# Optimization experiments

Measured on AMD Instinct MI355X. Metric: run time of the kernel, lower is better.

## Reference

```python
import jax, jax.numpy as jnp
import numpy as np

N_VAR, N_CONS = 100_000, 50_000
N_FEAS = N_VAR + N_CONS
E_OBJ, E_FEAS = 1_600_000, 2_400_000
H_OBJ = H_CONS = 64
C = H_OBJ + H_CONS  # concat_dim = 128
D = 256             # decoder_hidden_channels
NUM_GRAPHS = 64


def _gcn(x, src, dst, ew, W, b):
    # PyG GCNConv with edge weights: add self-loops (weight 1), sym-normalize, aggregate at dst.
    n = x.shape[0]
    loop = jnp.arange(n)
    src_f = jnp.concatenate([src, loop])
    dst_f = jnp.concatenate([dst, loop])
    ew_f = jnp.concatenate([ew, jnp.ones((n,), ew.dtype)])
    deg = jax.ops.segment_sum(ew_f, dst_f, num_segments=n)
    dinv = jnp.where(deg > 0, jax.lax.rsqrt(deg), 0.0)
    coef = dinv[src_f] * ew_f * dinv[dst_f]            # [E+n]
    h = x @ W                                          # [n, H]
    out = jax.ops.segment_sum(coef[:, None] * h[src_f], dst_f, num_segments=n)
    return out + b


def _mlp(z, W1, b1, W2, b2):
    return jnp.maximum(z @ W1 + b1, 0.0) @ W2 + b2


def setup_inputs() -> dict:
    key = jax.random.key(0)
    ks = iter(jax.random.split(key, 64))

    def nrm(shape, scale=1.0):
        return jax.random.normal(next(ks), shape, jnp.float32) * scale

    def lin(i, o):
        return nrm((i, o), 1.0 / np.sqrt(i)), jnp.zeros((o,), jnp.float32)

    inp = {}
    inp['x_obj'] = nrm((N_VAR, 4))
    inp['ei_obj'] = jax.random.randint(next(ks), (2, E_OBJ), 0, N_VAR)
    inp['ew_obj'] = jax.random.uniform(next(ks), (E_OBJ,), jnp.float32)
    inp['x_feas'] = nrm((N_FEAS, 4))
    inp['ei_feas'] = jax.random.randint(next(ks), (2, E_FEAS), 0, N_FEAS)
    inp['ew_feas'] = jax.random.uniform(next(ks), (E_FEAS,), jnp.float32)
    inp['batch_var'] = jnp.sort(jax.random.randint(next(ks), (N_VAR,), 0, NUM_GRAPHS))
    inp['n_var'] = N_VAR
    inp['n_bin'] = 50_000
    inp['c1o_W'], inp['c1o_b'] = lin(4, H_OBJ)
    inp['c2o_W'], inp['c2o_b'] = lin(H_OBJ, H_OBJ)
    inp['c1c_W'], inp['c1c_b'] = lin(4, H_CONS)
    inp['c2c_W'], inp['c2c_b'] = lin(H_CONS, H_CONS)
    inp['mu_W'], inp['mu_b'] = lin(C, C)
    inp['lv_W'], inp['lv_b'] = lin(C, C)
    inp['dx_W1'], inp['dx_b1'] = lin(C, D)
    inp['dx_W2'], inp['dx_b2'] = lin(D, 1)
    inp['dc_W1'], inp['dc_b1'] = lin(C, D)
    inp['dc_W2'], inp['dc_b2'] = lin(D, 1)
    inp['dk_W1'], inp['dk_b1'] = lin(C, D)
    inp['dk_W2'], inp['dk_b2'] = lin(D, 1)
    inp['di_W1'], inp['di_b1'] = lin(C, D)
    inp['di_W2'], inp['di_b2'] = lin(D, 1)
    return inp


def reference(x_obj, ei_obj, ew_obj, x_feas, ei_feas, ew_feas, batch_var, n_var, n_bin,
              c1o_W, c1o_b, c2o_W, c2o_b, c1c_W, c1c_b, c2c_W, c2c_b,
              mu_W, mu_b, lv_W, lv_b,
              dx_W1, dx_b1, dx_W2, dx_b2, dc_W1, dc_b1, dc_W2, dc_b2,
              dk_W1, dk_b1, dk_W2, dk_b2, di_W1, di_b1, di_W2, di_b2):
    so, do = ei_obj[0], ei_obj[1]
    sf, df = ei_feas[0], ei_feas[1]
    # objective encoder (all nodes are variables)
    h = jax.nn.relu(_gcn(x_obj, so, do, ew_obj, c1o_W, c1o_b))
    z_obj_var = jax.nn.relu(_gcn(h, so, do, ew_obj, c2o_W, c2o_b))
    # constraints encoder
    h = jax.nn.relu(_gcn(x_feas, sf, df, ew_feas, c1c_W, c1c_b))
    h = jax.nn.relu(_gcn(h, sf, df, ew_feas, c2c_W, c2c_b))
    z_cons_var = h[:n_var]          # variable_mask == first n_var nodes
    z_cons_constraints = h[n_var:]
    z_var = jnp.concatenate([z_obj_var, z_cons_var], axis=1)        # [N_var, C]
    z_cons_pad = jnp.pad(z_cons_constraints, ((0, 0), (0, C - z_cons_constraints.shape[1])))
    z_shared = jnp.concatenate([z_var, z_cons_pad], axis=0)         # [N_feas, C]
    z_mu = z_shared @ mu_W + mu_b
    z_logvar = z_shared @ lv_W + lv_b
    eps = jax.random.normal(jax.random.key(1), z_mu.shape, z_mu.dtype)
    z = z_mu + jnp.exp(0.5 * z_logvar) * eps
    z_var_s = z[:n_var]
    z_con_s = z[n_var:]
    x_hat = _mlp(z_var_s, dx_W1, dx_b1, dx_W2, dx_b2)[:, 0]
    # global_mean_pool over variable nodes
    sums = jax.ops.segment_sum(z_var_s, batch_var, num_segments=NUM_GRAPHS)
    cnts = jax.ops.segment_sum(jnp.ones((z_var_s.shape[0],), z.dtype), batch_var, num_segments=NUM_GRAPHS)
    pooled = sums / jnp.maximum(cnts, 1.0)[:, None]
    predicted_cost = _mlp(pooled, dc_W1, dc_b1, dc_W2, dc_b2)[:, 0]
    predicted_constraints = _mlp(z_con_s, dk_W1, dk_b1, dk_W2, dk_b2)[:, 0]
    integrality = jax.nn.sigmoid(_mlp(z_var_s, di_W1, di_b1, di_W2, di_b2))[:, 0]
    predicted_integrality = integrality[:n_bin]  # binary_mask == first n_bin variables
    return (x_hat, predicted_cost, predicted_constraints, predicted_integrality, z_mu, z_logvar)
```

## Files before the change

### kernel.cpp

```cpp
#include <hip/hip_runtime.h>
#include <math.h>

#define N_VAR_C  100000
#define N_CONS_C 50000
#define N_FEAS_C 150000
#define E_OBJ_C  1600000
#define E_FEAS_C 2400000
#define NG 64
#define N_BIN_C 50000
#define CAP 48

#define X_HAT_OFF 0
#define COST_OFF  100000
#define CONS_OFF  100064
#define INTG_OFF  150064
#define ZMU_OFF   200064
#define ZEL_TOTAL (N_FEAS_C * 128)
#define ZLV_OFF   (ZMU_OFF + ZEL_TOTAL)

typedef unsigned short u16;

static __device__ __forceinline__ float bf2f(u16 u) {
  return __uint_as_float(((unsigned)u) << 16);
}
static __device__ __forceinline__ u16 f2bf(float f) {
  unsigned x = __float_as_uint(f);
  unsigned r = x + 0x7FFFu + ((x >> 16) & 1u);
  return (u16)(r >> 16);
}

static __device__ __forceinline__ unsigned rotl32(unsigned x, unsigned r) {
  return (x << r) | (x >> (32u - r));
}

static __device__ __forceinline__ void threefry01(unsigned x0, unsigned x1,
                                                  unsigned& o0, unsigned& o1) {
  const unsigned ks0 = 0u, ks1 = 1u, ks2 = 0x1BD11BDAu ^ 0u ^ 1u;
  x0 += ks0; x1 += ks1;
  x0 += x1; x1 = rotl32(x1, 13); x1 ^= x0;
  x0 += x1; x1 = rotl32(x1, 15); x1 ^= x0;
  x0 += x1; x1 = rotl32(x1, 26); x1 ^= x0;
  x0 += x1; x1 = rotl32(x1, 6);  x1 ^= x0;
  x0 += ks1; x1 += ks2 + 1u;
  x0 += x1; x1 = rotl32(x1, 17); x1 ^= x0;
  x0 += x1; x1 = rotl32(x1, 29); x1 ^= x0;
  x0 += x1; x1 = rotl32(x1, 16); x1 ^= x0;
  x0 += x1; x1 = rotl32(x1, 24); x1 ^= x0;
  x0 += ks2; x1 += ks0 + 2u;
  x0 += x1; x1 = rotl32(x1, 13); x1 ^= x0;
  x0 += x1; x1 = rotl32(x1, 15); x1 ^= x0;
  x0 += x1; x1 = rotl32(x1, 26); x1 ^= x0;
  x0 += x1; x1 = rotl32(x1, 6);  x1 ^= x0;
  x0 += ks0; x1 += ks1 + 3u;
  x0 += x1; x1 = rotl32(x1, 17); x1 ^= x0;
  x0 += x1; x1 = rotl32(x1, 29); x1 ^= x0;
  x0 += x1; x1 = rotl32(x1, 16); x1 ^= x0;
  x0 += x1; x1 = rotl32(x1, 24); x1 ^= x0;
  x0 += ks1; x1 += ks2 + 4u;
  x0 += x1; x1 = rotl32(x1, 13); x1 ^= x0;
  x0 += x1; x1 = rotl32(x1, 15); x1 ^= x0;
  x0 += x1; x1 = rotl32(x1, 26); x1 ^= x0;
  x0 += x1; x1 = rotl32(x1, 6);  x1 ^= x0;
  x0 += ks2; x1 += ks0 + 5u;
  o0 = x0; o1 = x1;
}

static __device__ __forceinline__ float bits_to_normal(unsigned b) {
  float f = __uint_as_float(0x3F800000u | (b >> 9)) - 1.0f;
  const float lo = -0.99999994f;
  float u = f * 2.0f + lo;
  u = fmaxf(lo, u);
  float w = -log1pf(-u * u);
  float p;
  if (w < 5.0f) {
    w -= 2.5f;
    p = 2.81022636e-08f;
    p = fmaf(p, w, 3.43273939e-07f);
    p = fmaf(p, w, -3.5233877e-06f);
    p = fmaf(p, w, -4.39150654e-06f);
    p = fmaf(p, w, 0.00021858087f);
    p = fmaf(p, w, -0.00125372503f);
    p = fmaf(p, w, -0.00417768164f);
    p = fmaf(p, w, 0.246640727f);
    p = fmaf(p, w, 1.50140941f);
  } else {
    w = sqrtf(w) - 3.0f;
    p = -0.000200214257f;
    p = fmaf(p, w, 0.000100950558f);
    p = fmaf(p, w, 0.00134934322f);
    p = fmaf(p, w, -0.00367342844f);
    p = fmaf(p, w, 0.00573950773f);
    p = fmaf(p, w, -0.0076224613f);
    p = fmaf(p, w, 0.00943887047f);
    p = fmaf(p, w, 1.00167406f);
    p = fmaf(p, w, 2.83297682f);
  }
  return 1.41421354f * (p * u);
}

__global__ __launch_bounds__(256) void fill_slots_kernel(
    const int* __restrict__ src, const int* __restrict__ dst,
    const float* __restrict__ ew, int* __restrict__ cnt,
    int2* __restrict__ slots, int E) {
  int e = blockIdx.x * 256 + threadIdx.x;
  if (e >= E) return;
  int d = dst[e];
  int p = atomicAdd(&cnt[d], 1);
  if (p < CAP) slots[(size_t)d * CAP + p] = make_int2(src[e], __float_as_int(ew[e]));
}

__global__ __launch_bounds__(256) void deg_kernel(
    const int2* __restrict__ slots, const int* __restrict__ cnt,
    float* __restrict__ dinv, int n) {
  int node = blockIdx.x * 4 + (threadIdx.x >> 6);
  if (node >= n) return;
  int lane = threadIdx.x & 63;
  int c = min(cnt[node], CAP);
  float v = 0.f;
  if (lane < c) v = __int_as_float(slots[(size_t)node * CAP + lane].y);
  for (int off = 32; off >= 1; off >>= 1) v += __shfl_down(v, off, 64);
  if (lane == 0) dinv[node] = 1.0f / sqrtf(v + 1.0f);
}

__global__ __launch_bounds__(256) void coef_kernel(
    int2* __restrict__ slots, const int* __restrict__ cnt,
    const float* __restrict__ dinv, int n) {
  int idx = blockIdx.x * 256 + threadIdx.x;
  if (idx >= n * CAP) return;
  int node = idx / CAP;
  int p = idx - node * CAP;
  if (p >= min(cnt[node], CAP)) return;
  int2 s = slots[idx];
  float coef = dinv[s.x] * __int_as_float(s.y) * dinv[node];
  slots[idx].y = __float_as_int(coef);
}

__global__ __launch_bounds__(256) void xw4_kernel(
    const float* __restrict__ x, const float* __restrict__ W,
    u16* __restrict__ out, int n) {
  __shared__ float Ws[256];
  Ws[threadIdx.x] = W[threadIdx.x];
  __syncthreads();
  int gid = blockIdx.x * 256 + threadIdx.x;
  if (gid >= n * 64) return;
  int i = gid >> 6, c = gid & 63;
  float4 xv = *(const float4*)(x + i * 4);
  out[gid] = f2bf(xv.x * Ws[c] + xv.y * Ws[64 + c] + xv.z * Ws[128 + c] + xv.w * Ws[192 + c]);
}

__global__ __launch_bounds__(256) void gemm64_kernel(
    const float* __restrict__ h, const float* __restrict__ W,
    u16* __restrict__ out, int n) {
  __shared__ float Ws[4096];
  __shared__ float hs[1024];
  for (int i = threadIdx.x; i < 4096; i += 256) Ws[i] = W[i];
  int r0 = blockIdx.x * 16;
  for (int i = threadIdx.x; i < 1024; i += 256) {
    int r = r0 + (i >> 6);
    hs[i] = (r < n) ? h[(size_t)r * 64 + (i & 63)] : 0.f;
  }
  __syncthreads();
  int tx = threadIdx.x & 63, ty = threadIdx.x >> 6;
  float a0 = 0, a1 = 0, a2 = 0, a3 = 0;
  for (int k = 0; k < 64; ++k) {
    float w = Ws[k * 64 + tx];
    a0 = fmaf(hs[ty * 64 + k], w, a0);
    a1 = fmaf(hs[(ty + 4) * 64 + k], w, a1);
    a2 = fmaf(hs[(ty + 8) * 64 + k], w, a2);
    a3 = fmaf(hs[(ty + 12) * 64 + k], w, a3);
  }
  int r = r0 + ty;
  if (r < n) out[(size_t)r * 64 + tx] = f2bf(a0);
  r += 4; if (r < n) out[(size_t)r * 64 + tx] = f2bf(a1);
  r += 4; if (r < n) out[(size_t)r * 64 + tx] = f2bf(a2);
  r += 4; if (r < n) out[(size_t)r * 64 + tx] = f2bf(a3);
}

__global__ __launch_bounds__(256) void agg_kernel(
    const u16* __restrict__ t, const float* __restrict__ dinv,
    const int* __restrict__ cnt, const int2* __restrict__ slots,
    const float* __restrict__ bias, float* __restrict__ out, int n) {
  int node = blockIdx.x * 4 + (threadIdx.x >> 6);
  if (node >= n) return;
  int lane = threadIdx.x & 63;
  int half = lane >> 5;
  int cc = (lane & 31) * 2;
  float di = dinv[node];
  float acc0 = 0.f, acc1 = 0.f;
  if (half == 0) {
    unsigned v = *(const unsigned*)(t + (size_t)node * 64 + cc);
    acc0 = bias[cc]     + di * di * bf2f((u16)(v & 0xffffu));
    acc1 = bias[cc + 1] + di * di * bf2f((u16)(v >> 16));
  }
  const int2* sl = slots + (size_t)node * CAP;
  int pe = min(cnt[node], CAP);
  int p = half;
  for (; p + 6 < pe; p += 8) {
    int2 s0 = sl[p];
    int2 s1 = sl[p + 2];
    int2 s2 = sl[p + 4];
    int2 s3 = sl[p + 6];
    unsigned v0 = *(const unsigned*)(t + (size_t)s0.x * 64 + cc);
    unsigned v1 = *(const unsigned*)(t + (size_t)s1.x * 64 + cc);
    unsigned v2 = *(const unsigned*)(t + (size_t)s2.x * 64 + cc);
    unsigned v3 = *(const unsigned*)(t + (size_t)s3.x * 64 + cc);
    float w0 = __int_as_float(s0.y), w1 = __int_as_float(s1.y);
    float w2 = __int_as_float(s2.y), w3 = __int_as_float(s3.y);
    acc0 = fmaf(w0, bf2f((u16)(v0 & 0xffffu)), acc0);
    acc1 = fmaf(w0, bf2f((u16)(v0 >> 16)), acc1);
    acc0 = fmaf(w1, bf2f((u16)(v1 & 0xffffu)), acc0);
    acc1 = fmaf(w1, bf2f((u16)(v1 >> 16)), acc1);
    acc0 = fmaf(w2, bf2f((u16)(v2 & 0xffffu)), acc0);
    acc1 = fmaf(w2, bf2f((u16)(v2 >> 16)), acc1);
    acc0 = fmaf(w3, bf2f((u16)(v3 & 0xffffu)), acc0);
    acc1 = fmaf(w3, bf2f((u16)(v3 >> 16)), acc1);
  }
  for (; p < pe; p += 2) {
    int2 s = sl[p];
    unsigned v = *(const unsigned*)(t + (size_t)s.x * 64 + cc);
    float w = __int_as_float(s.y);
    acc0 = fmaf(w, bf2f((u16)(v & 0xffffu)), acc0);
    acc1 = fmaf(w, bf2f((u16)(v >> 16)), acc1);
  }
  acc0 += __shfl_xor(acc0, 32, 64);
  acc1 += __shfl_xor(acc1, 32, 64);
  if (half == 0) {
    float2 o = make_float2(fmaxf(acc0, 0.f), fmaxf(acc1, 0.f));
    *(float2*)(out + (size_t)node * 64 + cc) = o;
  }
}

__global__ __launch_bounds__(128) void mulv_kernel(
    const float* __restrict__ zobj, const float* __restrict__ hfeas,
    const float* __restrict__ muW, const float* __restrict__ mub,
    const float* __restrict__ lvW, const float* __restrict__ lvb,
    float* __restrict__ zmu, float* __restrict__ zlv) {
  int r0 = blockIdx.x * 8;
  int j = threadIdx.x;
  bool isvar = (r0 < N_VAR_C);
  float am[8], al[8];
  float mb = mub[j], lb = lvb[j];
#pragma unroll
  for (int r = 0; r < 8; ++r) { am[r] = mb; al[r] = lb; }
  const float* u0 = isvar ? zobj : hfeas;
  for (int k = 0; k < 64; ++k) {
    float wm = muW[k * 128 + j], wl = lvW[k * 128 + j];
#pragma unroll
    for (int r = 0; r < 8; ++r) {
      float zv = u0[(size_t)(r0 + r) * 64 + k];
      am[r] = fmaf(zv, wm, am[r]);
      al[r] = fmaf(zv, wl, al[r]);
    }
  }
  if (isvar) {
    for (int k = 0; k < 64; ++k) {
      float wm = muW[(64 + k) * 128 + j], wl = lvW[(64 + k) * 128 + j];
#pragma unroll
      for (int r = 0; r < 8; ++r) {
        float zv = hfeas[(size_t)(r0 + r) * 64 + k];
        am[r] = fmaf(zv, wm, am[r]);
        al[r] = fmaf(zv, wl, al[r]);
      }
    }
  }
#pragma unroll
  for (int r = 0; r < 8; ++r) {
    zmu[(size_t)(r0 + r) * 128 + j] = am[r];
    zlv[(size_t)(r0 + r) * 128 + j] = al[r];
  }
}

__global__ __launch_bounds__(256) void zgen_kernel(
    const float* __restrict__ zmu, const float* __restrict__ zlv, float* __restrict__ z) {
  int j = blockIdx.x * 256 + threadIdx.x;
  if (j >= ZEL_TOTAL) return;
  unsigned o0, o1;
  threefry01(0u, (unsigned)j, o0, o1);
  float e = bits_to_normal(o0 ^ o1);
  z[j] = fmaf(expf(0.5f * zlv[j]), e, zmu[j]);
}

#define POOL_ROWS 128
__global__ __launch_bounds__(256) void pool_accum_kernel(
    const float* __restrict__ z, const int* __restrict__ batch,
    float* __restrict__ sums, int* __restrict__ cnts) {
  int c = threadIdx.x & 127;
  int rsub = threadIdx.x >> 7;
  int r0 = blockIdx.x * POOL_ROWS;
  int rend = min(r0 + POOL_ROWS, N_VAR_C);
  float acc = 0.f;
  int cnt = 0;
  int cur = -1;
  for (int r = r0 + rsub; r < rend; r += 2) {
    int g = batch[r];
    if (g != cur) {
      if (cnt > 0) {
        atomicAdd(&sums[cur * 128 + c], acc);
        if (c == 0) atomicAdd(&cnts[cur], cnt);
      }
      acc = 0.f; cnt = 0; cur = g;
    }
    acc += z[(size_t)r * 128 + c];
    cnt++;
  }
  if (cnt > 0) {
    atomicAdd(&sums[cur * 128 + c], acc);
    if (c == 0) atomicAdd(&cnts[cur], cnt);
  }
}

__global__ __launch_bounds__(256) void pool_final_kernel(
    const float* __restrict__ sums, const int* __restrict__ cnts,
    float* __restrict__ pooled) {
  int i = blockIdx.x * 256 + threadIdx.x;
  if (i >= NG * 128) return;
  float cnt = (float)cnts[i >> 7];
  pooled[i] = sums[i] / fmaxf(cnt, 1.0f);
}

__global__ __launch_bounds__(128) void mlp_kernel(
    const float* __restrict__ in, const float* __restrict__ W1,
    const float* __restrict__ b1, const float* __restrict__ W2,
    const float* __restrict__ b2, float* __restrict__ out,
    int n, int rowoff, int sigmoid_out) {
  __shared__ float red[128];
  int r0 = blockIdx.x * 8;
  int j = threadIdx.x;
  float a0[8], a1[8];
  float b1a = b1[j], b1b = b1[j + 128];
#pragma unroll
  for (int r = 0; r < 8; ++r) { a0[r] = b1a; a1[r] = b1b; }
  const float* base = in + (size_t)(rowoff + r0) * 128;
  for (int k = 0; k < 128; ++k) {
    float w0 = W1[k * 256 + j], w1 = W1[k * 256 + 128 + j];
#pragma unroll
    for (int r = 0; r < 8; ++r) {
      float zv = base[r * 128 + k];
      a0[r] = fmaf(zv, w0, a0[r]);
      a1[r] = fmaf(zv, w1, a1[r]);
    }
  }
  float w2a = W2[j], w2b = W2[j + 128], bias2 = b2[0];
  for (int r = 0; r < 8; ++r) {
    float hv = fmaxf(a0[r], 0.f) * w2a + fmaxf(a1[r], 0.f) * w2b;
    red[j] = hv;
    __syncthreads();
    for (int off = 64; off >= 1; off >>= 1) {
      if (j < off) red[j] += red[j + off];
      __syncthreads();
    }
    if (j == 0 && (r0 + r) < n) {
      float o = red[0] + bias2;
      if (sigmoid_out) o = 1.0f / (1.0f + expf(-o));
      out[r0 + r] = o;
    }
    __syncthreads();
  }
}

extern "C" void kernel_launch(void* const* d_in, const int* in_sizes, int n_in,
                              void* d_out, int out_size, void* d_ws, size_t ws_size,
                              hipStream_t stream) {
  const float* x_obj   = (const float*)d_in[0];
  const int*   ei_obj  = (const int*)d_in[1];
  const float* ew_obj  = (const float*)d_in[2];
  const float* x_feas  = (const float*)d_in[3];
  const int*   ei_feas = (const int*)d_in[4];
  const float* ew_feas = (const float*)d_in[5];
  const int*   batch   = (const int*)d_in[6];
  const float* c1o_W = (const float*)d_in[9];
  const float* c1o_b = (const float*)d_in[10];
  const float* c2o_W = (const float*)d_in[11];
  const float* c2o_b = (const float*)d_in[12];
  const float* c1c_W = (const float*)d_in[13];
  const float* c1c_b = (const float*)d_in[14];
  const float* c2c_W = (const float*)d_in[15];
  const float* c2c_b = (const float*)d_in[16];
  const float* mu_W  = (const float*)d_in[17];
  const float* mu_b  = (const float*)d_in[18];
  const float* lv_W  = (const float*)d_in[19];
  const float* lv_b  = (const float*)d_in[20];
  const float* dx_W1 = (const float*)d_in[21];
  const float* dx_b1 = (const float*)d_in[22];
  const float* dx_W2 = (const float*)d_in[23];
  const float* dx_b2 = (const float*)d_in[24];
  const float* dc_W1 = (const float*)d_in[25];
  const float* dc_b1 = (const float*)d_in[26];
  const float* dc_W2 = (const float*)d_in[27];
  const float* dc_b2 = (const float*)d_in[28];
  const float* dk_W1 = (const float*)d_in[29];
  const float* dk_b1 = (const float*)d_in[30];
  const float* dk_W2 = (const float*)d_in[31];
  const float* dk_b2 = (const float*)d_in[32];
  const float* di_W1 = (const float*)d_in[33];
  const float* di_b1 = (const float*)d_in[34];
  const float* di_W2 = (const float*)d_in[35];
  const float* di_b2 = (const float*)d_in[36];

  float* out = (float*)d_out;
  char* ws = (char*)d_ws;
  size_t off = 0;
  auto alloc = [&](size_t bytes) -> char* {
    char* p = ws + off;
    off = (off + bytes + 255) & ~(size_t)255;
    return p;
  };

  float* Z = (float*)alloc(sizeof(float) * (size_t)N_FEAS_C * 128);
  float* B = Z;
  float* ZOBJ = Z + (size_t)N_FEAS_C * 64;
  u16* T = (u16*)alloc(sizeof(u16) * (size_t)N_FEAS_C * 64);
  int2* slots = (int2*)alloc(sizeof(int2) * (size_t)N_FEAS_C * CAP);
  float* dinv_o = (float*)alloc(sizeof(float) * N_VAR_C);
  float* dinv_f = (float*)alloc(sizeof(float) * N_FEAS_C);
  int* cnt_o = (int*)alloc(sizeof(int) * N_VAR_C);
  int* cnt_f = (int*)alloc(sizeof(int) * N_FEAS_C);
  float* psum   = (float*)alloc(sizeof(float) * NG * 128);
  int*   pcnt   = (int*)alloc(sizeof(int) * NG);
  float* pooled = (float*)alloc(sizeof(float) * NG * 128);

  float* zmu_out = out + ZMU_OFF;
  float* zlv_out = out + ZLV_OFF;

  const int* src_obj  = ei_obj;
  const int* dst_obj  = ei_obj + E_OBJ_C;
  const int* src_feas = ei_feas;
  const int* dst_feas = ei_feas + E_FEAS_C;

  hipMemsetAsync(cnt_o, 0, sizeof(int) * N_VAR_C, stream);
  hipMemsetAsync(cnt_f, 0, sizeof(int) * N_FEAS_C, stream);
  hipMemsetAsync(psum, 0, sizeof(float) * NG * 128, stream);
  hipMemsetAsync(pcnt, 0, sizeof(int) * NG, stream);

  fill_slots_kernel<<<(E_OBJ_C + 255) / 256, 256, 0, stream>>>(src_obj, dst_obj, ew_obj, cnt_o, slots, E_OBJ_C);
  deg_kernel<<<N_VAR_C / 4, 256, 0, stream>>>(slots, cnt_o, dinv_o, N_VAR_C);
  coef_kernel<<<(N_VAR_C * CAP + 255) / 256, 256, 0, stream>>>(slots, cnt_o, dinv_o, N_VAR_C);

  xw4_kernel<<<(N_VAR_C * 64 + 255) / 256, 256, 0, stream>>>(x_obj, c1o_W, T, N_VAR_C);
  agg_kernel<<<N_VAR_C / 4, 256, 0, stream>>>(T, dinv_o, cnt_o, slots, c1o_b, B, N_VAR_C);
  gemm64_kernel<<<N_VAR_C / 16, 256, 0, stream>>>(B, c2o_W, T, N_VAR_C);
  agg_kernel<<<N_VAR_C / 4, 256, 0, stream>>>(T, dinv_o, cnt_o, slots, c2o_b, ZOBJ, N_VAR_C);

  fill_slots_kernel<<<(E_FEAS_C + 255) / 256, 256, 0, stream>>>(src_feas, dst_feas, ew_feas, cnt_f, slots, E_FEAS_C);
  deg_kernel<<<N_FEAS_C / 4, 256, 0, stream>>>(slots, cnt_f, dinv_f, N_FEAS_C);
  coef_kernel<<<(N_FEAS_C * CAP + 255) / 256, 256, 0, stream>>>(slots, cnt_f, dinv_f, N_FEAS_C);

  xw4_kernel<<<(N_FEAS_C * 64 + 255) / 256, 256, 0, stream>>>(x_feas, c1c_W, T, N_FEAS_C);
  agg_kernel<<<N_FEAS_C / 4, 256, 0, stream>>>(T, dinv_f, cnt_f, slots, c1c_b, B, N_FEAS_C);
  gemm64_kernel<<<N_FEAS_C / 16, 256, 0, stream>>>(B, c2c_W, T, N_FEAS_C);
  agg_kernel<<<N_FEAS_C / 4, 256, 0, stream>>>(T, dinv_f, cnt_f, slots, c2c_b, B, N_FEAS_C);

  mulv_kernel<<<N_FEAS_C / 8, 128, 0, stream>>>(ZOBJ, B, mu_W, mu_b, lv_W, lv_b, zmu_out, zlv_out);

  zgen_kernel<<<(ZEL_TOTAL + 255) / 256, 256, 0, stream>>>(zmu_out, zlv_out, Z);

  pool_accum_kernel<<<(N_VAR_C + POOL_ROWS - 1) / POOL_ROWS, 256, 0, stream>>>(Z, batch, psum, pcnt);
  pool_final_kernel<<<(NG * 128 + 255) / 256, 256, 0, stream>>>(psum, pcnt, pooled);

  mlp_kernel<<<N_VAR_C / 8, 128, 0, stream>>>(Z, dx_W1, dx_b1, dx_W2, dx_b2, out + X_HAT_OFF, N_VAR_C, 0, 0);
  mlp_kernel<<<(NG + 7) / 8, 128, 0, stream>>>(pooled, dc_W1, dc_b1, dc_W2, dc_b2, out + COST_OFF, NG, 0, 0);
  mlp_kernel<<<N_CONS_C / 8, 128, 0, stream>>>(Z, dk_W1, dk_b1, dk_W2, dk_b2, out + CONS_OFF, N_CONS_C, N_VAR_C, 0);
  mlp_kernel<<<N_BIN_C / 8, 128, 0, stream>>>(Z, di_W1, di_b1, di_W2, di_b2, out + INTG_OFF, N_BIN_C, 0, 1);
}
```

Measured before the change: 1.349 ms.

## Fuse first GCN layer by aggregating raw 4-dim features and applying W inline

Replaces the separate x@W kernel plus aggregation of 64-wide bf16 hidden rows with one kernel. It gathers the 4-float input rows of neighbours and computes x·W on the fly per edge, using the 16 weights held in registers. Each gathered row is 16 bytes instead of a 128-byte bf16 row, and the T intermediate write and read go away. The cost is redundant per-edge matmul arithmetic. Accumulation is now fp32 rather than through bf16 rounding, and the ReLU is applied here, presumably matching what agg_kernel did for layer one.

```diff
diff --git a/kernel.cpp b/kernel.cpp
--- a/kernel.cpp
+++ b/kernel.cpp
@@ -135,17 +135,65 @@
   slots[idx].y = __float_as_int(coef);
 }
 
-__global__ __launch_bounds__(256) void xw4_kernel(
+__global__ __launch_bounds__(256) void agg1_kernel(
     const float* __restrict__ x, const float* __restrict__ W,
-    u16* __restrict__ out, int n) {
-  __shared__ float Ws[256];
-  Ws[threadIdx.x] = W[threadIdx.x];
-  __syncthreads();
-  int gid = blockIdx.x * 256 + threadIdx.x;
-  if (gid >= n * 64) return;
-  int i = gid >> 6, c = gid & 63;
-  float4 xv = *(const float4*)(x + i * 4);
-  out[gid] = f2bf(xv.x * Ws[c] + xv.y * Ws[64 + c] + xv.z * Ws[128 + c] + xv.w * Ws[192 + c]);
+    const float* __restrict__ dinv, const int* __restrict__ cnt,
+    const int2* __restrict__ slots, const float* __restrict__ bias,
+    float* __restrict__ out, int n) {
+  int node = blockIdx.x * 4 + (threadIdx.x >> 6);
+  if (node >= n) return;
+  int lane = threadIdx.x & 63;
+  int half = lane >> 5;
+  int cc = (lane & 31) * 2;
+  float w00 = W[cc],       w01 = W[cc + 1];
+  float w10 = W[64 + cc],  w11 = W[64 + cc + 1];
+  float w20 = W[128 + cc], w21 = W[128 + cc + 1];
+  float w30 = W[192 + cc], w31 = W[192 + cc + 1];
+  float di = dinv[node];
+  float acc0 = 0.f, acc1 = 0.f;
+  if (half == 0) {
+    float4 xv = *(const float4*)(x + (size_t)node * 4);
+    float h0 = xv.x * w00 + xv.y * w10 + xv.z * w20 + xv.w * w30;
+    float h1 = xv.x * w01 + xv.y * w11 + xv.z * w21 + xv.w * w31;
+    acc0 = bias[cc]     + di * di * h0;
+    acc1 = bias[cc + 1] + di * di * h1;
+  }
+  const int2* sl = slots + (size_t)node * CAP;
+  int pe = min(cnt[node], CAP);
+  int p = half;
+  for (; p + 6 < pe; p += 8) {
+    int2 s0 = sl[p];
+    int2 s1 = sl[p + 2];
+    int2 s2 = sl[p + 4];
+    int2 s3 = sl[p + 6];
+    float4 x0 = *(const float4*)(x + (size_t)s0.x * 4);
+    float4 x1 = *(const float4*)(x + (size_t)s1.x * 4);
+    float4 x2 = *(const float4*)(x + (size_t)s2.x * 4);
+    float4 x3 = *(const float4*)(x + (size_t)s3.x * 4);
+    float w0 = __int_as_float(s0.y), w1 = __int_as_float(s1.y);
+    float w2 = __int_as_float(s2.y), w3 = __int_as_float(s3.y);
+    acc0 = fmaf(w0, x0.x * w00 + x0.y * w10 + x0.z * w20 + x0.w * w30, acc0);
+    acc1 = fmaf(w0, x0.x * w01 + x0.y * w11 + x0.z * w21 + x0.w * w31, acc1);
+    acc0 = fmaf(w1, x1.x * w00 + x1.y * w10 + x1.z * w20 + x1.w * w30, acc0);
+    acc1 = fmaf(w1, x1.x * w01 + x1.y * w11 + x1.z * w21 + x1.w * w31, acc1);
+    acc0 = fmaf(w2, x2.x * w00 + x2.y * w10 + x2.z * w20 + x2.w * w30, acc0);
+    acc1 = fmaf(w2, x2.x * w01 + x2.y * w11 + x2.z * w21 + x2.w * w31, acc1);
+    acc0 = fmaf(w3, x3.x * w00 + x3.y * w10 + x3.z * w20 + x3.w * w30, acc0);
+    acc1 = fmaf(w3, x3.x * w01 + x3.y * w11 + x3.z * w21 + x3.w * w31, acc1);
+  }
+  for (; p < pe; p += 2) {
+    int2 s = sl[p];
+    float4 xv = *(const float4*)(x + (size_t)s.x * 4);
+    float w = __int_as_float(s.y);
+    acc0 = fmaf(w, xv.x * w00 + xv.y * w10 + xv.z * w20 + xv.w * w30, acc0);
+    acc1 = fmaf(w, xv.x * w01 + xv.y * w11 + xv.z * w21 + xv.w * w31, acc1);
+  }
+  acc0 += __shfl_xor(acc0, 32, 64);
+  acc1 += __shfl_xor(acc1, 32, 64);
+  if (half == 0) {
+    float2 o = make_float2(fmaxf(acc0, 0.f), fmaxf(acc1, 0.f));
+    *(float2*)(out + (size_t)node * 64 + cc) = o;
+  }
 }
 
 __global__ __launch_bounds__(256) void gemm64_kernel(
@@ -436,8 +484,7 @@
   deg_kernel<<<N_VAR_C / 4, 256, 0, stream>>>(slots, cnt_o, dinv_o, N_VAR_C);
   coef_kernel<<<(N_VAR_C * CAP + 255) / 256, 256, 0, stream>>>(slots, cnt_o, dinv_o, N_VAR_C);
 
-  xw4_kernel<<<(N_VAR_C * 64 + 255) / 256, 256, 0, stream>>>(x_obj, c1o_W, T, N_VAR_C);
-  agg_kernel<<<N_VAR_C / 4, 256, 0, stream>>>(T, dinv_o, cnt_o, slots, c1o_b, B, N_VAR_C);
+  agg1_kernel<<<N_VAR_C / 4, 256, 0, stream>>>(x_obj, c1o_W, dinv_o, cnt_o, slots, c1o_b, B, N_VAR_C);
   gemm64_kernel<<<N_VAR_C / 16, 256, 0, stream>>>(B, c2o_W, T, N_VAR_C);
   agg_kernel<<<N_VAR_C / 4, 256, 0, stream>>>(T, dinv_o, cnt_o, slots, c2o_b, ZOBJ, N_VAR_C);
 
@@ -445,8 +492,7 @@
   deg_kernel<<<N_FEAS_C / 4, 256, 0, stream>>>(slots, cnt_f, dinv_f, N_FEAS_C);
   coef_kernel<<<(N_FEAS_C * CAP + 255) / 256, 256, 0, stream>>>(slots, cnt_f, dinv_f, N_FEAS_C);
 
-  xw4_kernel<<<(N_FEAS_C * 64 + 255) / 256, 256, 0, stream>>>(x_feas, c1c_W, T, N_FEAS_C);
-  agg_kernel<<<N_FEAS_C / 4, 256, 0, stream>>>(T, dinv_f, cnt_f, slots, c1c_b, B, N_FEAS_C);
+  agg1_kernel<<<N_FEAS_C / 4, 256, 0, stream>>>(x_feas, c1c_W, dinv_f, cnt_f, slots, c1c_b, B, N_FEAS_C);
   gemm64_kernel<<<N_FEAS_C / 16, 256, 0, stream>>>(B, c2c_W, T, N_FEAS_C);
   agg_kernel<<<N_FEAS_C / 4, 256, 0, stream>>>(T, dinv_f, cnt_f, slots, c2c_b, B, N_FEAS_C);
 
```

Measured after the change: 1.344 ms. About the same (-0.4%).
